# Performance work log

Measured on AMD Instinct MI355X. Metric: run time of the kernel, lower is better.

The kernel has to match this reference:

```python
import jax, jax.numpy as jnp
import numpy as np

L, D, H, FF, V = 8, 768, 8, 2048, 32000
MAXLEN, TMAX = 512, 4
S = MAXLEN * TMAX  # 2048 context length
HD = D // H
EPS = 1e-4  # layer_norm_eps from module defaults


def setup_inputs() -> dict:
    key = jax.random.key(0)
    ks = jax.random.split(key, 16)
    s = 0.02
    B = 1
    rn = lambda k, shape: jax.random.normal(k, shape, jnp.float32) * s
    # sinusoidal positional encoding over MAXLEN real-token positions
    pos = np.arange(MAXLEN)[:, None]
    div = np.exp(np.arange(0, D, 2) * (-np.log(10000.0) / D))
    pe = np.zeros((MAXLEN, D), np.float32)
    pe[:, 0::2] = np.sin(pos * div)
    pe[:, 1::2] = np.cos(pos * div)
    return {
        "state_embeddings": jax.random.normal(ks[0], (B, S, D), jnp.float32),
        "padding_mask": jnp.zeros((B, S), bool),
        "pe": jnp.asarray(pe),
        "thought_emb": rn(ks[1], (TMAX, D)),
        "w_qkv": rn(ks[2], (L, 3 * D, D)),
        "b_qkv": jnp.zeros((L, 3 * D), jnp.float32),
        "w_out": rn(ks[3], (L, D, D)),
        "b_out": jnp.zeros((L, D), jnp.float32),
        "ln1_g": jnp.ones((L, D), jnp.float32),
        "ln1_b": jnp.zeros((L, D), jnp.float32),
        "ln2_g": jnp.ones((L, D), jnp.float32),
        "ln2_b": jnp.zeros((L, D), jnp.float32),
        "w_ff1": rn(ks[4], (L, FF, D)),
        "b_ff1": jnp.zeros((L, FF), jnp.float32),
        "w_ff2": rn(ks[5], (L, D, FF)),
        "b_ff2": jnp.zeros((L, D), jnp.float32),
        "fn_g": jnp.ones((D,), jnp.float32),
        "fn_b": jnp.zeros((D,), jnp.float32),
        "w_policy": rn(ks[6], (V, D)),
        "w_v1": rn(ks[7], (FF, D)),
        "b_v1": jnp.zeros((FF,), jnp.float32),
        "w_v2": rn(ks[8], (1, FF)),
        "b_v2": jnp.zeros((1,), jnp.float32),
        "n_thoughts_taken": 3,
    }


def _layer_norm(x, g, b):
    m = x.mean(-1, keepdims=True)
    v = ((x - m) ** 2).mean(-1, keepdims=True)
    return (x - m) / jnp.sqrt(v + EPS) * g + b


def reference(state_embeddings, padding_mask, pe, thought_emb, w_qkv, b_qkv, w_out, b_out, ln1_g, ln1_b, ln2_g, ln2_b, w_ff1, b_ff1, w_ff2, b_ff2, fn_g, fn_b, w_policy, w_v1, b_v1, w_v2, b_v2, n_thoughts_taken):
    tt = int(n_thoughts_taken)
    T = tt + 1  # block size (token + thoughts taken)
    B = state_embeddings.shape[0]
    R = MAXLEN  # real_token_count: all token slots real (no padding)
    # --- DualPositionalEncoding ---
    x = state_embeddings[:, :MAXLEN * T].reshape(B, MAXLEN, T, D)
    x = x + pe[None, :, None, :] + thought_emb[None, None, :T, :]
    x = x.reshape(B, MAXLEN * T, D)
    x = jnp.pad(x, ((0, 0), (0, S - MAXLEN * T), (0, 0)))
    # --- ThoughtsFormer block-causal mask (keep=True means attend) ---
    i = jnp.arange(S)
    tok, off = i // T, i % T
    same_block = (tok[:, None] == tok[None, :]) & (off[:, None] >= off[None, :]) & (tok[:, None] < R)
    global_cols = (off[None, :] == 0) & (tok[None, :] < R) & (i[:, None] > i[None, :]) & (i[:, None] < R * T)
    keep = (same_block | global_cols)[None, None] & (~padding_mask)[:, None, None, :]
    scale = 1.0 / np.sqrt(HD)

    def layer(h, p):
        wq, bq, wo, bo, g1, b1, g2, b2, wf1, bf1, wf2, bf2 = p
        # pre-norm self-attention
        y = _layer_norm(h, g1, b1)
        q, k, v = jnp.split(y @ wq.T + bq, 3, axis=-1)
        q = q.reshape(B, S, H, HD)
        k = k.reshape(B, S, H, HD)
        v = v.reshape(B, S, H, HD)
        scores = jnp.einsum('bihd,bjhd->bhij', q, k) * scale
        attn = jax.nn.softmax(jnp.where(keep, scores, -jnp.inf), axis=-1)
        o = jnp.einsum('bhij,bjhd->bihd', attn, v).reshape(B, S, D)
        h = h + o @ wo.T + bo
        # pre-norm FFN with exact (erf) GELU
        y = _layer_norm(h, g2, b2)
        h = h + jax.nn.gelu(y @ wf1.T + bf1, approximate=False) @ wf2.T + bf2
        h = jnp.where(jnp.isnan(h), 0.0, h)
        return h, None

    x, _ = jax.lax.scan(layer, x, (w_qkv, b_qkv, w_out, b_out, ln1_g, ln1_b, ln2_g, ln2_b, w_ff1, b_ff1, w_ff2, b_ff2))
    x = _layer_norm(x, fn_g, fn_b)  # TransformerEncoder final norm
    logits = x @ w_policy.T  # policy head (no bias)
    values = jax.nn.gelu(x @ w_v1.T + b_v1, approximate=False) @ w_v2.T + b_v2
    return logits, values
```

## Files before the change

kernel.cpp:

```cpp
#include <hip/hip_runtime.h>
#include <math.h>

#define S_TOT 2048
#define DMODEL 768
#define QKVD 2304
#define NHEAD 8
#define HDIM 96
#define FFDIM 2048
#define VOCAB 32000
#define MAXLEN_C 512
#define POL_CHUNK 3200
#define VLT_LD 2080
#define NEG_BIG (-3.0e38f)
#define M_INIT (-1.0e30f)
#define QK_SCALE 0.10206207261596575f

typedef __bf16 bf16x8 __attribute__((ext_vector_type(8)));
typedef float f32x4 __attribute__((ext_vector_type(4)));
typedef unsigned short u16x8 __attribute__((ext_vector_type(8)));
typedef unsigned short u16x4 __attribute__((ext_vector_type(4)));

__device__ __forceinline__ float gelu_exact(float x) {
  return 0.5f * x * (1.0f + erff(x * 0.70710678118654752f));
}

__device__ __forceinline__ float bf2f(unsigned short u) {
  union { unsigned int i; float f; } v;
  v.i = ((unsigned int)u) << 16;
  return v.f;
}

__device__ __forceinline__ unsigned short f2bf(float f) {
  union { float f; unsigned int i; } v;
  v.f = f;
  unsigned int x = v.i;
  return (unsigned short)((x + 0x7fffu + ((x >> 16) & 1u)) >> 16);
}

__device__ __forceinline__ unsigned int pack2bf(float a, float b) {
  return (unsigned int)f2bf(a) | ((unsigned int)f2bf(b) << 16);
}

__device__ __forceinline__ void gload_lds16(const unsigned short* g, unsigned short* l) {
  __builtin_amdgcn_global_load_lds(
      (const __attribute__((address_space(1))) unsigned int*)g,
      (__attribute__((address_space(3))) unsigned int*)l, 16, 0, 0);
}

__global__ __launch_bounds__(256) void embed_kernel(
    const float* __restrict__ se, const float* __restrict__ pe,
    const float* __restrict__ th, const int* __restrict__ ntt,
    float* __restrict__ X) {
  int idx = blockIdx.x * 256 + threadIdx.x;
  if (idx >= S_TOT * DMODEL) return;
  int p = idx / DMODEL;
  int d = idx - p * DMODEL;
  int T = ntt[0] + 1;
  float v = 0.0f;
  if (p < MAXLEN_C * T) {
    v = se[idx] + pe[(p / T) * DMODEL + d] + th[(p % T) * DMODEL + d];
  }
  X[idx] = v;
}

__global__ __launch_bounds__(256) void ln_bf_kernel(
    const float* __restrict__ X, const float* __restrict__ g,
    const float* __restrict__ b, unsigned short* __restrict__ Y) {
  __shared__ float red[4];
  const int row = blockIdx.x;
  const int tid = threadIdx.x;
  const float* x = X + (size_t)row * DMODEL;
  float v0 = x[tid], v1 = x[tid + 256], v2 = x[tid + 512];
  float s = v0 + v1 + v2;
  for (int o = 32; o; o >>= 1) s += __shfl_xor(s, o);
  if ((tid & 63) == 0) red[tid >> 6] = s;
  __syncthreads();
  float mean = (red[0] + red[1] + red[2] + red[3]) * (1.0f / DMODEL);
  float d0 = v0 - mean, d1 = v1 - mean, d2 = v2 - mean;
  float s2 = d0 * d0 + d1 * d1 + d2 * d2;
  for (int o = 32; o; o >>= 1) s2 += __shfl_xor(s2, o);
  __syncthreads();
  if ((tid & 63) == 0) red[tid >> 6] = s2;
  __syncthreads();
  float var = (red[0] + red[1] + red[2] + red[3]) * (1.0f / DMODEL);
  float rstd = rsqrtf(var + 1e-4f);
  unsigned short* y = Y + (size_t)row * DMODEL;
  y[tid]       = f2bf(d0 * rstd * g[tid]       + b[tid]);
  y[tid + 256] = f2bf(d1 * rstd * g[tid + 256] + b[tid + 256]);
  y[tid + 512] = f2bf(d2 * rstd * g[tid + 512] + b[tid + 512]);
}

__global__ __launch_bounds__(256) void cvt_kernel(
    const float* __restrict__ s, unsigned short* __restrict__ d, int n) {
  int i = (blockIdx.x * 256 + threadIdx.x) * 4;
  if (i >= n) return;
  float4 v = *(const float4*)(s + i);
  u16x4 o;
  o[0] = f2bf(v.x); o[1] = f2bf(v.y); o[2] = f2bf(v.z); o[3] = f2bf(v.w);
  *(u16x4*)(d + i) = o;
}

__global__ __launch_bounds__(256) void cvt4_kernel(
    const float* __restrict__ s0, const float* __restrict__ s1,
    const float* __restrict__ s2, const float* __restrict__ s3,
    unsigned short* __restrict__ d0, unsigned short* __restrict__ d1,
    unsigned short* __restrict__ d2, unsigned short* __restrict__ d3,
    int n0, int n1, int n2, int n3) {
  int i = (blockIdx.x * 256 + threadIdx.x) * 4;
  const float* s;
  unsigned short* d;
  if (i < n0) { s = s0; d = d0; }
  else if (i < n0 + n1) { i -= n0; s = s1; d = d1; }
  else if (i < n0 + n1 + n2) { i -= n0 + n1; s = s2; d = d2; }
  else if (i < n0 + n1 + n2 + n3) { i -= n0 + n1 + n2; s = s3; d = d3; }
  else return;
  float4 v = *(const float4*)(s + i);
  u16x4 o;
  o[0] = f2bf(v.x); o[1] = f2bf(v.y); o[2] = f2bf(v.z); o[3] = f2bf(v.w);
  *(u16x4*)(d + i) = o;
}

__global__ __launch_bounds__(256) void cvt6_kernel(
    const float* __restrict__ s0, const float* __restrict__ s1,
    const float* __restrict__ s2, const float* __restrict__ s3,
    const float* __restrict__ s4, const float* __restrict__ s5,
    unsigned short* __restrict__ d0, unsigned short* __restrict__ d1,
    unsigned short* __restrict__ d2, unsigned short* __restrict__ d3,
    unsigned short* __restrict__ d4, unsigned short* __restrict__ d5,
    int n0, int n1, int n2, int n3, int n4, int n5) {
  int i = (blockIdx.x * 256 + threadIdx.x) * 4;
  const float* s;
  unsigned short* d;
  if (i < n0) { s = s0; d = d0; }
  else if (i < n0 + n1) { i -= n0; s = s1; d = d1; }
  else if (i < n0 + n1 + n2) { i -= n0 + n1; s = s2; d = d2; }
  else if (i < n0 + n1 + n2 + n3) { i -= n0 + n1 + n2; s = s3; d = d3; }
  else if (i < n0 + n1 + n2 + n3 + n4) { i -= n0 + n1 + n2 + n3; s = s4; d = d4; }
  else if (i < n0 + n1 + n2 + n3 + n4 + n5) { i -= n0 + n1 + n2 + n3 + n4; s = s5; d = d5; }
  else return;
  float4 v = *(const float4*)(s + i);
  u16x4 o;
  o[0] = f2bf(v.x); o[1] = f2bf(v.y); o[2] = f2bf(v.z); o[3] = f2bf(v.w);
  *(u16x4*)(d + i) = o;
}

__global__ __launch_bounds__(256) void gemm_bf16_kernel(
    const unsigned short* __restrict__ A, const unsigned short* __restrict__ B,
    const float* __restrict__ bias, const float* __restrict__ res,
    void* __restrict__ Cout, int M, int N, int K, int ldc, int act, int outbf) {
  __shared__ __align__(16) unsigned short As[128 * 32];
  __shared__ __align__(16) unsigned short Bs[128 * 32];
  const int t = threadIdx.x;
  const int w = t >> 6, l = t & 63;
  const int n0 = blockIdx.x * 128, i0 = blockIdx.y * 128;
  const int wr = w >> 1, wc = w & 1;
  const int lr = l & 15;
  const int koff = (l >> 4) * 8;

  f32x4 acc[4][4] = {};

  const int srow = t >> 2;
  const int scol = (t & 3) * 8;
  const unsigned short* Ag = A + (size_t)(i0 + srow) * K + scol;
  const unsigned short* Bg = B + (size_t)(n0 + srow) * K + scol;
  unsigned short* Alds0 = &As[(w << 9)];
  unsigned short* Alds1 = &As[2048 + (w << 9)];
  unsigned short* Blds0 = &Bs[(w << 9)];
  unsigned short* Blds1 = &Bs[2048 + (w << 9)];

  for (int k0 = 0; k0 < K; k0 += 32) {
    __syncthreads();
    gload_lds16(Ag + k0, Alds0);
    gload_lds16(Ag + (size_t)64 * K + k0, Alds1);
    gload_lds16(Bg + k0, Blds0);
    gload_lds16(Bg + (size_t)64 * K + k0, Blds1);
    __syncthreads();

    bf16x8 af[4], bfr[4];
#pragma unroll
    for (int fi = 0; fi < 4; ++fi)
      af[fi] = *(const bf16x8*)&As[(wr * 64 + fi * 16 + lr) * 32 + koff];
#pragma unroll
    for (int fj = 0; fj < 4; ++fj)
      bfr[fj] = *(const bf16x8*)&Bs[(wc * 64 + fj * 16 + lr) * 32 + koff];
#pragma unroll
    for (int fi = 0; fi < 4; ++fi)
#pragma unroll
      for (int fj = 0; fj < 4; ++fj)
        acc[fi][fj] = __builtin_amdgcn_mfma_f32_16x16x32_bf16(
            af[fi], bfr[fj], acc[fi][fj], 0, 0, 0);
  }

  float bcol[4];
#pragma unroll
  for (int fj = 0; fj < 4; ++fj)
    bcol[fj] = bias ? bias[n0 + wc * 64 + fj * 16 + lr] : 0.0f;

#pragma unroll
  for (int fi = 0; fi < 4; ++fi) {
#pragma unroll
    for (int reg = 0; reg < 4; ++reg) {
      const int i = i0 + wr * 64 + fi * 16 + (l >> 4) * 4 + reg;
      const size_t rowbase = (size_t)i * ldc;
#pragma unroll
      for (int fj = 0; fj < 4; ++fj) {
        const int n = n0 + wc * 64 + fj * 16 + lr;
        float z = acc[fi][fj][reg] + bcol[fj];
        if (act) z = gelu_exact(z);
        if (res) z += res[rowbase + n];
        if (outbf) ((unsigned short*)Cout)[rowbase + n] = f2bf(z);
        else       ((float*)Cout)[rowbase + n] = z;
      }
    }
  }
}

__global__ __launch_bounds__(256) void gemm64_bf16_kernel(
    const unsigned short* __restrict__ A, const unsigned short* __restrict__ B,
    const float* __restrict__ bias, const float* __restrict__ res,
    void* __restrict__ Cout, int M, int N, int K, int ldc, int act, int outbf) {
  __shared__ __align__(16) unsigned short As[2 * 64 * 32];
  __shared__ __align__(16) unsigned short Bs[2 * 64 * 32];
  const int t = threadIdx.x;
  const int w = t >> 6, l = t & 63;
  const int n0 = blockIdx.x * 64, i0 = blockIdx.y * 64;
  const int wr = w >> 1, wc = w & 1;
  const int lr = l & 15;
  const int koff = (l >> 4) * 8;

  f32x4 acc[2][2] = {};

  const int srow = t >> 2;
  const int scol = (t & 3) * 8;
  const unsigned short* Ag = A + (size_t)(i0 + srow) * K + scol;
  const unsigned short* Bg = B + (size_t)(n0 + srow) * K + scol;
  unsigned short* Alds0 = &As[(w << 9)];
  unsigned short* Alds1 = &As[2048 + (w << 9)];
  unsigned short* Blds0 = &Bs[(w << 9)];
  unsigned short* Blds1 = &Bs[2048 + (w << 9)];

  for (int k0 = 0; k0 < K; k0 += 64) {
    __syncthreads();
    gload_lds16(Ag + k0, Alds0);
    gload_lds16(Ag + k0 + 32, Alds1);
    gload_lds16(Bg + k0, Blds0);
    gload_lds16(Bg + k0 + 32, Blds1);
    __syncthreads();

    bf16x8 af[2][2], bfr[2][2];
#pragma unroll
    for (int fi = 0; fi < 2; ++fi)
#pragma unroll
      for (int kk = 0; kk < 2; ++kk)
        af[fi][kk] = *(const bf16x8*)&As[kk * 2048 + (wr * 32 + fi * 16 + lr) * 32 + koff];
#pragma unroll
    for (int fj = 0; fj < 2; ++fj)
#pragma unroll
      for (int kk = 0; kk < 2; ++kk)
        bfr[fj][kk] = *(const bf16x8*)&Bs[kk * 2048 + (wc * 32 + fj * 16 + lr) * 32 + koff];
#pragma unroll
    for (int fi = 0; fi < 2; ++fi)
#pragma unroll
      for (int fj = 0; fj < 2; ++fj)
#pragma unroll
        for (int kk = 0; kk < 2; ++kk)
          acc[fi][fj] = __builtin_amdgcn_mfma_f32_16x16x32_bf16(
              af[fi][kk], bfr[fj][kk], acc[fi][fj], 0, 0, 0);
  }

  float bcol[2];
#pragma unroll
  for (int fj = 0; fj < 2; ++fj)
    bcol[fj] = bias ? bias[n0 + wc * 32 + fj * 16 + lr] : 0.0f;

#pragma unroll
  for (int fi = 0; fi < 2; ++fi) {
#pragma unroll
    for (int reg = 0; reg < 4; ++reg) {
      const int i = i0 + wr * 32 + fi * 16 + (l >> 4) * 4 + reg;
      const size_t rowbase = (size_t)i * ldc;
#pragma unroll
      for (int fj = 0; fj < 2; ++fj) {
        const int n = n0 + wc * 32 + fj * 16 + lr;
        float z = acc[fi][fj][reg] + bcol[fj];
        if (act) z = gelu_exact(z);
        if (res) z += res[rowbase + n];
        if (outbf) ((unsigned short*)Cout)[rowbase + n] = f2bf(z);
        else       ((float*)Cout)[rowbase + n] = z;
      }
    }
  }
}

__global__ __launch_bounds__(256) void repack_kernel(
    const unsigned short* __restrict__ qkv, const int* __restrict__ ntt,
    unsigned short* __restrict__ Kg, unsigned short* __restrict__ Vgt,
    unsigned short* __restrict__ Vlt) {
  __shared__ unsigned short vt[64][104];
  const int pb = blockIdx.x * 64, h = blockIdx.y;
  const int T = ntt[0] + 1;
  const int tid = threadIdx.x;

  for (int idx = tid; idx < 64 * 96; idx += 256) {
    int pp = idx / 96, d = idx - pp * 96;
    vt[pp][d] = qkv[(size_t)(pb + pp) * QKVD + 2 * DMODEL + h * HDIM + d];
  }
  const int firstpp = (T - pb % T) % T;
  const int ng = (64 - firstpp + T - 1) / T;
  for (int idx = tid; idx < ng * 96; idx += 256) {
    int gi = idx / 96, d = idx - gi * 96;
    int p = pb + firstpp + gi * T;
    int g = p / T;
    if (g < MAXLEN_C)
      Kg[((size_t)h * 512 + g) * 96 + d] = qkv[(size_t)p * QKVD + DMODEL + h * HDIM + d];
  }
  __syncthreads();
  for (int idx = tid; idx < 96 * 64; idx += 256) {
    int d = idx >> 6, pp = idx & 63;
    Vlt[((size_t)h * 96 + d) * VLT_LD + pb + pp] = vt[pp][d];
  }
  for (int idx = tid; idx < ng * 96; idx += 256) {
    int d = idx / ng, gi = idx - d * ng;
    int pp = firstpp + gi * T;
    int g = (pb + pp) / T;
    if (g < MAXLEN_C && d < 96)
      Vgt[((size_t)h * 96 + d) * 512 + g] = vt[pp][d];
  }
}

__global__ __launch_bounds__(256) void attn_flash_kernel(
    const unsigned short* __restrict__ qkv, const unsigned short* __restrict__ Kg,
    const unsigned short* __restrict__ Vgt, const unsigned short* __restrict__ Vlt,
    const int* __restrict__ ntt, unsigned short* __restrict__ att) {
  __shared__ float Osh[4][96][17];
  __shared__ float Msh[4][16];
  __shared__ float Lsh[4][16];
  const int s = blockIdx.x, h = blockIdx.y;
  const int T = ntt[0] + 1;
  const int tid = threadIdx.x;
  const int w = tid >> 6, l = tid & 63;
  const int q15 = l & 15, grp = l >> 4;
  const int p0 = s * 16;
  const int p = p0 + q15;
  const int myTok = p / T;

  const unsigned short* qrow = qkv + (size_t)p * QKVD + h * HDIM + grp * 8;
  bf16x8 qf0 = *(const bf16x8*)(qrow);
  bf16x8 qf1 = *(const bf16x8*)(qrow + 32);
  bf16x8 qf2 = *(const bf16x8*)(qrow + 64);

  float m_run = M_INIT, l_run = 0.0f;
  f32x4 oacc[6] = {};

  const int gmax = (p0 + 15) / T;
  const int KP = (gmax >> 5) + 1;
  const unsigned short* KgH = Kg + (size_t)h * 512 * 96;
  const unsigned short* VgH = Vgt + (size_t)h * 96 * 512;

  for (int kp = w; kp < KP; kp += 4) {
    f32x4 s0 = {}, s1 = {};
    const unsigned short* k0r = KgH + (size_t)(kp * 32 + q15) * 96 + grp * 8;
    const unsigned short* k1r = k0r + 16 * 96;
    {
      bf16x8 a0 = *(const bf16x8*)(k0r);
      bf16x8 a1 = *(const bf16x8*)(k1r);
      s0 = __builtin_amdgcn_mfma_f32_16x16x32_bf16(a0, qf0, s0, 0, 0, 0);
      s1 = __builtin_amdgcn_mfma_f32_16x16x32_bf16(a1, qf0, s1, 0, 0, 0);
      a0 = *(const bf16x8*)(k0r + 32);
      a1 = *(const bf16x8*)(k1r + 32);
      s0 = __builtin_amdgcn_mfma_f32_16x16x32_bf16(a0, qf1, s0, 0, 0, 0);
      s1 = __builtin_amdgcn_mfma_f32_16x16x32_bf16(a1, qf1, s1, 0, 0, 0);
      a0 = *(const bf16x8*)(k0r + 64);
      a1 = *(const bf16x8*)(k1r + 64);
      s0 = __builtin_amdgcn_mfma_f32_16x16x32_bf16(a0, qf2, s0, 0, 0, 0);
      s1 = __builtin_amdgcn_mfma_f32_16x16x32_bf16(a1, qf2, s1, 0, 0, 0);
    }
    float sc[8];
#pragma unroll
    for (int e = 0; e < 4; ++e) {
      int g = kp * 32 + grp * 4 + e;
      sc[e] = (g * T <= p) ? s0[e] * QK_SCALE : NEG_BIG;
      g += 16;
      sc[4 + e] = (g * T <= p) ? s1[e] * QK_SCALE : NEG_BIG;
    }
    float tmax = sc[0];
#pragma unroll
    for (int e = 1; e < 8; ++e) tmax = fmaxf(tmax, sc[e]);
    tmax = fmaxf(tmax, __shfl_xor(tmax, 16));
    tmax = fmaxf(tmax, __shfl_xor(tmax, 32));
    float mnew = fmaxf(m_run, tmax);
    float alpha = __expf(m_run - mnew);
    float pv[8], ps = 0.0f;
#pragma unroll
    for (int e = 0; e < 8; ++e) { pv[e] = __expf(sc[e] - mnew); ps += pv[e]; }
    ps += __shfl_xor(ps, 16);
    ps += __shfl_xor(ps, 32);
    l_run = l_run * alpha + ps;
    m_run = mnew;
#pragma unroll
    for (int dt = 0; dt < 6; ++dt) oacc[dt] *= alpha;
    unsigned int pk0[2], pk1[2];
    pk0[0] = pack2bf(pv[0], pv[1]); pk0[1] = pack2bf(pv[2], pv[3]);
    pk1[0] = pack2bf(pv[4], pv[5]); pk1[1] = pack2bf(pv[6], pv[7]);
    union { unsigned int u[4]; bf16x8 v; } pf;
#pragma unroll
    for (int w2 = 0; w2 < 4; ++w2) {
      int src = (((grp & 1) << 1) + (w2 >> 1)) * 16 + q15;
      int y0 = __shfl((int)pk0[w2 & 1], src);
      int y1 = __shfl((int)pk1[w2 & 1], src);
      pf.u[w2] = (grp >> 1) ? (unsigned int)y1 : (unsigned int)y0;
    }
#pragma unroll
    for (int dt = 0; dt < 6; ++dt) {
      bf16x8 vf = *(const bf16x8*)(VgH + (size_t)(dt * 16 + q15) * 512 + kp * 32 + grp * 8);
      oacc[dt] = __builtin_amdgcn_mfma_f32_16x16x32_bf16(vf, pf.v, oacc[dt], 0, 0, 0);
    }
  }

  if (w == 3) {
    f32x4 s0 = {};
    const unsigned short* kl = qkv + (size_t)(p0 + q15) * QKVD + DMODEL + h * HDIM + grp * 8;
    s0 = __builtin_amdgcn_mfma_f32_16x16x32_bf16(*(const bf16x8*)(kl), qf0, s0, 0, 0, 0);
    s0 = __builtin_amdgcn_mfma_f32_16x16x32_bf16(*(const bf16x8*)(kl + 32), qf1, s0, 0, 0, 0);
    s0 = __builtin_amdgcn_mfma_f32_16x16x32_bf16(*(const bf16x8*)(kl + 64), qf2, s0, 0, 0, 0);
    float sc[4];
#pragma unroll
    for (int e = 0; e < 4; ++e) {
      int pk = p0 + grp * 4 + e;
      bool ok = (pk / T == myTok) && (pk % T != 0) && (pk <= p);
      sc[e] = ok ? s0[e] * QK_SCALE : NEG_BIG;
    }
    float tmax = fmaxf(fmaxf(sc[0], sc[1]), fmaxf(sc[2], sc[3]));
    tmax = fmaxf(tmax, __shfl_xor(tmax, 16));
    tmax = fmaxf(tmax, __shfl_xor(tmax, 32));
    float mnew = fmaxf(m_run, tmax);
    float alpha = __expf(m_run - mnew);
    float pv[4], ps = 0.0f;
#pragma unroll
    for (int e = 0; e < 4; ++e) { pv[e] = __expf(sc[e] - mnew); ps += pv[e]; }
    ps += __shfl_xor(ps, 16);
    ps += __shfl_xor(ps, 32);
    l_run = l_run * alpha + ps;
    m_run = mnew;
#pragma unroll
    for (int dt = 0; dt < 6; ++dt) oacc[dt] *= alpha;
    unsigned int pk0[2];
    pk0[0] = pack2bf(pv[0], pv[1]); pk0[1] = pack2bf(pv[2], pv[3]);
    union { unsigned int u[4]; bf16x8 v; } pf;
#pragma unroll
    for (int w2 = 0; w2 < 4; ++w2) {
      int src = (((grp & 1) << 1) + (w2 >> 1)) * 16 + q15;
      int y0 = __shfl((int)pk0[w2 & 1], src);
      pf.u[w2] = (grp >> 1) ? 0u : (unsigned int)y0;
    }
#pragma unroll
    for (int dt = 0; dt < 6; ++dt) {
      bf16x8 vf = *(const bf16x8*)(Vlt + ((size_t)h * 96 + dt * 16 + q15) * VLT_LD + p0 + grp * 8);
      oacc[dt] = __builtin_amdgcn_mfma_f32_16x16x32_bf16(vf, pf.v, oacc[dt], 0, 0, 0);
    }
  }

  if (l < 16) { Msh[w][l] = m_run; Lsh[w][l] = l_run; }
#pragma unroll
  for (int dt = 0; dt < 6; ++dt)
#pragma unroll
    for (int e = 0; e < 4; ++e)
      Osh[w][dt * 16 + grp * 4 + e][q15] = oacc[dt][e];
  __syncthreads();

  {
    const int q = tid & 15, dg = tid >> 4;
    float m0 = Msh[0][q], m1 = Msh[1][q], m2 = Msh[2][q], m3 = Msh[3][q];
    float ms = fmaxf(fmaxf(m0, m1), fmaxf(m2, m3));
    float c0 = __expf(m0 - ms), c1 = __expf(m1 - ms);
    float c2 = __expf(m2 - ms), c3 = __expf(m3 - ms);
    float lsum = c0 * Lsh[0][q] + c1 * Lsh[1][q] + c2 * Lsh[2][q] + c3 * Lsh[3][q];
    float rinv = 1.0f / lsum;
    unsigned short* orow = att + (size_t)(p0 + q) * DMODEL + h * HDIM;
#pragma unroll
    for (int j = 0; j < 6; ++j) {
      int d = dg * 6 + j;
      float o = c0 * Osh[0][d][q] + c1 * Osh[1][d][q] +
                c2 * Osh[2][d][q] + c3 * Osh[3][d][q];
      orow[d] = f2bf(o * rinv);
    }
  }
}

__global__ __launch_bounds__(256) void v2_kernel(
    const unsigned short* __restrict__ F1, const float* __restrict__ w2,
    const float* __restrict__ b2, float* __restrict__ out) {
  __shared__ float red[4];
  const int row = blockIdx.x;
  const int tid = threadIdx.x;
  float s = 0.0f;
  const unsigned short* xr = F1 + (size_t)row * FFDIM;
  for (int f = tid; f < FFDIM; f += 256) s += bf2f(xr[f]) * w2[f];
  for (int o = 32; o; o >>= 1) s += __shfl_xor(s, o);
  if ((tid & 63) == 0) red[tid >> 6] = s;
  __syncthreads();
  if (tid == 0) out[row] = red[0] + red[1] + red[2] + red[3] + b2[0];
}

extern "C" void kernel_launch(void* const* d_in, const int* in_sizes, int n_in,
                              void* d_out, int out_size, void* d_ws, size_t ws_size,
                              hipStream_t stream) {
  const float* se      = (const float*)d_in[0];
  const float* pe      = (const float*)d_in[2];
  const float* th      = (const float*)d_in[3];
  const float* w_qkv   = (const float*)d_in[4];
  const float* b_qkv   = (const float*)d_in[5];
  const float* w_out   = (const float*)d_in[6];
  const float* b_out   = (const float*)d_in[7];
  const float* ln1_g   = (const float*)d_in[8];
  const float* ln1_b   = (const float*)d_in[9];
  const float* ln2_g   = (const float*)d_in[10];
  const float* ln2_b   = (const float*)d_in[11];
  const float* w_ff1   = (const float*)d_in[12];
  const float* b_ff1   = (const float*)d_in[13];
  const float* w_ff2   = (const float*)d_in[14];
  const float* b_ff2   = (const float*)d_in[15];
  const float* fn_g    = (const float*)d_in[16];
  const float* fn_b    = (const float*)d_in[17];
  const float* w_pol   = (const float*)d_in[18];
  const float* w_v1    = (const float*)d_in[19];
  const float* b_v1    = (const float*)d_in[20];
  const float* w_v2    = (const float*)d_in[21];
  const float* b_v2    = (const float*)d_in[22];
  const int*   ntt     = (const int*)d_in[23];

  float* logits = (float*)d_out;
  float* values = logits + (size_t)S_TOT * VOCAB;

  const int nq = 3 * DMODEL * DMODEL, no = DMODEL * DMODEL;
  const int nf1 = FFDIM * DMODEL, nf2 = DMODEL * FFDIM;
  const int npol = VOCAB * DMODEL;

  char* p = (char*)d_ws;
  float* X             = (float*)p;          p += (size_t)S_TOT * DMODEL * 4;
  unsigned short* Ybf  = (unsigned short*)p; p += (size_t)S_TOT * DMODEL * 2;
  unsigned short* QKVb = (unsigned short*)p; p += (size_t)S_TOT * QKVD * 2;
  unsigned short* ATTb = (unsigned short*)p; p += (size_t)S_TOT * DMODEL * 2;
  unsigned short* F1b  = (unsigned short*)p; p += (size_t)S_TOT * FFDIM * 2;
  unsigned short* Kg   = (unsigned short*)p; p += (size_t)NHEAD * 512 * 96 * 2;
  unsigned short* Vgt  = (unsigned short*)p; p += (size_t)NHEAD * 96 * 512 * 2;
  unsigned short* Vlt  = (unsigned short*)p; p += (size_t)NHEAD * 96 * VLT_LD * 2;

  const size_t wbytes = ((size_t)8 * (nq + no + nf1 + nf2) + npol + nf1) * 2;
  const size_t used   = (size_t)(p - (char*)d_ws);
  const bool bigws = ws_size >= used + wbytes + (1u << 20);

  unsigned short *WqA, *WoA, *Wf1A, *Wf2A, *WpolA, *Wv1A;
  if (bigws) {
    WqA   = (unsigned short*)p; p += (size_t)8 * nq * 2;
    WoA   = (unsigned short*)p; p += (size_t)8 * no * 2;
    Wf1A  = (unsigned short*)p; p += (size_t)8 * nf1 * 2;
    Wf2A  = (unsigned short*)p; p += (size_t)8 * nf2 * 2;
    WpolA = (unsigned short*)p; p += (size_t)npol * 2;
    Wv1A  = (unsigned short*)p;
  } else {
    WqA   = (unsigned short*)p; p += (size_t)nq * 2;
    WoA   = (unsigned short*)p; p += (size_t)no * 2;
    Wf1A  = (unsigned short*)p; p += (size_t)nf1 * 2;
    Wf2A  = (unsigned short*)p; p += (size_t)nf2 * 2;
    WpolA = (unsigned short*)p;
    Wv1A  = Wf1A;
  }

  dim3 blk(256);

  if (bigws) {
    const int t0 = 8 * nq, t1 = 8 * no, t2 = 8 * nf1, t3 = 8 * nf2;
    const long total = (long)t0 + t1 + t2 + t3 + npol + nf1;
    cvt6_kernel<<<dim3((unsigned)((total / 4 + 255) / 256)), blk, 0, stream>>>(
        w_qkv, w_out, w_ff1, w_ff2, w_pol, w_v1,
        WqA, WoA, Wf1A, Wf2A, WpolA, Wv1A,
        t0, t1, t2, t3, npol, nf1);
  }

  embed_kernel<<<dim3((S_TOT * DMODEL + 255) / 256), blk, 0, stream>>>(se, pe, th, ntt, X);

  for (int l = 0; l < 8; ++l) {
    const unsigned short* pWq  = bigws ? WqA  + (size_t)l * nq  : WqA;
    const unsigned short* pWo  = bigws ? WoA  + (size_t)l * no  : WoA;
    const unsigned short* pWf1 = bigws ? Wf1A + (size_t)l * nf1 : Wf1A;
    const unsigned short* pWf2 = bigws ? Wf2A + (size_t)l * nf2 : Wf2A;
    if (!bigws) {
      const int ncvt4 = (nq + no + nf1 + nf2) / 4;
      cvt4_kernel<<<dim3((ncvt4 + 255) / 256), blk, 0, stream>>>(
          w_qkv + (size_t)l * nq, w_out + (size_t)l * no,
          w_ff1 + (size_t)l * nf1, w_ff2 + (size_t)l * nf2,
          WqA, WoA, Wf1A, Wf2A, nq, no, nf1, nf2);
    }

    ln_bf_kernel<<<dim3(S_TOT), blk, 0, stream>>>(X, ln1_g + l * DMODEL, ln1_b + l * DMODEL, Ybf);
    gemm_bf16_kernel<<<dim3(QKVD / 128, S_TOT / 128), blk, 0, stream>>>(
        Ybf, pWq, b_qkv + (size_t)l * 3 * DMODEL, nullptr, QKVb,
        S_TOT, QKVD, DMODEL, QKVD, 0, 1);
    repack_kernel<<<dim3(S_TOT / 64, NHEAD), blk, 0, stream>>>(QKVb, ntt, Kg, Vgt, Vlt);
    attn_flash_kernel<<<dim3(S_TOT / 16, NHEAD), blk, 0, stream>>>(
        QKVb, Kg, Vgt, Vlt, ntt, ATTb);
    gemm64_bf16_kernel<<<dim3(DMODEL / 64, S_TOT / 64), blk, 0, stream>>>(
        ATTb, pWo, b_out + (size_t)l * DMODEL, X, X,
        S_TOT, DMODEL, DMODEL, DMODEL, 0, 0);

    ln_bf_kernel<<<dim3(S_TOT), blk, 0, stream>>>(X, ln2_g + l * DMODEL, ln2_b + l * DMODEL, Ybf);
    gemm_bf16_kernel<<<dim3(FFDIM / 128, S_TOT / 128), blk, 0, stream>>>(
        Ybf, pWf1, b_ff1 + (size_t)l * FFDIM, nullptr, F1b,
        S_TOT, FFDIM, DMODEL, FFDIM, 1, 1);
    gemm64_bf16_kernel<<<dim3(DMODEL / 64, S_TOT / 64), blk, 0, stream>>>(
        F1b, pWf2, b_ff2 + (size_t)l * DMODEL, X, X,
        S_TOT, DMODEL, FFDIM, DMODEL, 0, 0);
  }

  ln_bf_kernel<<<dim3(S_TOT), blk, 0, stream>>>(X, fn_g, fn_b, Ybf);

  if (bigws) {
    gemm_bf16_kernel<<<dim3(VOCAB / 128, S_TOT / 128), blk, 0, stream>>>(
        Ybf, WpolA, nullptr, nullptr, logits, S_TOT, VOCAB, DMODEL, VOCAB, 0, 0);
  } else {
    for (int c = 0; c < VOCAB / POL_CHUNK; ++c) {
      cvt_kernel<<<dim3((POL_CHUNK * DMODEL / 4 + 255) / 256), blk, 0, stream>>>(
          w_pol + (size_t)c * POL_CHUNK * DMODEL, WpolA, POL_CHUNK * DMODEL);
      gemm_bf16_kernel<<<dim3(POL_CHUNK / 128, S_TOT / 128), blk, 0, stream>>>(
          Ybf, WpolA, nullptr, nullptr, logits + (size_t)c * POL_CHUNK,
          S_TOT, POL_CHUNK, DMODEL, VOCAB, 0, 0);
    }
  }

  if (!bigws)
    cvt_kernel<<<dim3((nf1 / 4 + 255) / 256), blk, 0, stream>>>(w_v1, Wv1A, nf1);
  gemm_bf16_kernel<<<dim3(FFDIM / 128, S_TOT / 128), blk, 0, stream>>>(
      Ybf, Wv1A, b_v1, nullptr, F1b, S_TOT, FFDIM, DMODEL, FFDIM, 1, 1);
  v2_kernel<<<dim3(S_TOT), blk, 0, stream>>>(F1b, w_v2, b_v2, values);
}
```

Measured before the change: 1.517 ms.

## Swizzle policy GEMM blocks across XCDs and prioritize MFMA in attention

The policy-head GEMM now runs on a 1D grid and remaps block IDs so consecutive blocks assigned round-robin to the 8 XCDs cover contiguous M-tiles of the same N column, which should improve L2 reuse of the weight and activation tiles. In the flash-attention kernel, all K fragment loads are hoisted ahead of the QK MFMAs, and s_setprio raises wave priority around the MFMA sequences to favour matrix issue over other waves. The swizzle hardcodes 16 M-tiles and assumes the grid divides by 8. The priority hints may help or hurt scheduling depending on occupancy.

```diff
diff --git a/kernel.cpp b/kernel.cpp
--- a/kernel.cpp
+++ b/kernel.cpp
@@ -147,12 +147,23 @@
 __global__ __launch_bounds__(256) void gemm_bf16_kernel(
     const unsigned short* __restrict__ A, const unsigned short* __restrict__ B,
     const float* __restrict__ bias, const float* __restrict__ res,
-    void* __restrict__ Cout, int M, int N, int K, int ldc, int act, int outbf) {
+    void* __restrict__ Cout, int M, int N, int K, int ldc, int act, int outbf,
+    int swiz) {
   __shared__ __align__(16) unsigned short As[128 * 32];
   __shared__ __align__(16) unsigned short Bs[128 * 32];
   const int t = threadIdx.x;
   const int w = t >> 6, l = t & 63;
-  const int n0 = blockIdx.x * 128, i0 = blockIdx.y * 128;
+  int n_blk, m_blk;
+  if (swiz) {
+    const int g = blockIdx.x;
+    const int chunk = gridDim.x >> 3;
+    const int logical = (g & 7) * chunk + (g >> 3);
+    m_blk = logical & 15;
+    n_blk = logical >> 4;
+  } else {
+    n_blk = blockIdx.x; m_blk = blockIdx.y;
+  }
+  const int n0 = n_blk * 128, i0 = m_blk * 128;
   const int wr = w >> 1, wc = w & 1;
   const int lr = l & 15;
   const int koff = (l >> 4) * 8;
@@ -364,16 +375,18 @@
     {
       bf16x8 a0 = *(const bf16x8*)(k0r);
       bf16x8 a1 = *(const bf16x8*)(k1r);
+      bf16x8 b0 = *(const bf16x8*)(k0r + 32);
+      bf16x8 b1 = *(const bf16x8*)(k1r + 32);
+      bf16x8 c0 = *(const bf16x8*)(k0r + 64);
+      bf16x8 c1 = *(const bf16x8*)(k1r + 64);
+      __builtin_amdgcn_s_setprio(1);
       s0 = __builtin_amdgcn_mfma_f32_16x16x32_bf16(a0, qf0, s0, 0, 0, 0);
       s1 = __builtin_amdgcn_mfma_f32_16x16x32_bf16(a1, qf0, s1, 0, 0, 0);
-      a0 = *(const bf16x8*)(k0r + 32);
-      a1 = *(const bf16x8*)(k1r + 32);
-      s0 = __builtin_amdgcn_mfma_f32_16x16x32_bf16(a0, qf1, s0, 0, 0, 0);
-      s1 = __builtin_amdgcn_mfma_f32_16x16x32_bf16(a1, qf1, s1, 0, 0, 0);
-      a0 = *(const bf16x8*)(k0r + 64);
-      a1 = *(const bf16x8*)(k1r + 64);
-      s0 = __builtin_amdgcn_mfma_f32_16x16x32_bf16(a0, qf2, s0, 0, 0, 0);
-      s1 = __builtin_amdgcn_mfma_f32_16x16x32_bf16(a1, qf2, s1, 0, 0, 0);
+      s0 = __builtin_amdgcn_mfma_f32_16x16x32_bf16(b0, qf1, s0, 0, 0, 0);
+      s1 = __builtin_amdgcn_mfma_f32_16x16x32_bf16(b1, qf1, s1, 0, 0, 0);
+      s0 = __builtin_amdgcn_mfma_f32_16x16x32_bf16(c0, qf2, s0, 0, 0, 0);
+      s1 = __builtin_amdgcn_mfma_f32_16x16x32_bf16(c1, qf2, s1, 0, 0, 0);
+      __builtin_amdgcn_s_setprio(0);
     }
     float sc[8];
 #pragma unroll
@@ -410,19 +423,23 @@
       int y1 = __shfl((int)pk1[w2 & 1], src);
       pf.u[w2] = (grp >> 1) ? (unsigned int)y1 : (unsigned int)y0;
     }
+    __builtin_amdgcn_s_setprio(1);
 #pragma unroll
     for (int dt = 0; dt < 6; ++dt) {
       bf16x8 vf = *(const bf16x8*)(VgH + (size_t)(dt * 16 + q15) * 512 + kp * 32 + grp * 8);
       oacc[dt] = __builtin_amdgcn_mfma_f32_16x16x32_bf16(vf, pf.v, oacc[dt], 0, 0, 0);
     }
+    __builtin_amdgcn_s_setprio(0);
   }
 
   if (w == 3) {
     f32x4 s0 = {};
     const unsigned short* kl = qkv + (size_t)(p0 + q15) * QKVD + DMODEL + h * HDIM + grp * 8;
+    __builtin_amdgcn_s_setprio(1);
     s0 = __builtin_amdgcn_mfma_f32_16x16x32_bf16(*(const bf16x8*)(kl), qf0, s0, 0, 0, 0);
     s0 = __builtin_amdgcn_mfma_f32_16x16x32_bf16(*(const bf16x8*)(kl + 32), qf1, s0, 0, 0, 0);
     s0 = __builtin_amdgcn_mfma_f32_16x16x32_bf16(*(const bf16x8*)(kl + 64), qf2, s0, 0, 0, 0);
+    __builtin_amdgcn_s_setprio(0);
     float sc[4];
 #pragma unroll
     for (int e = 0; e < 4; ++e) {
@@ -453,11 +470,13 @@
       int y0 = __shfl((int)pk0[w2 & 1], src);
       pf.u[w2] = (grp >> 1) ? 0u : (unsigned int)y0;
     }
+    __builtin_amdgcn_s_setprio(1);
 #pragma unroll
     for (int dt = 0; dt < 6; ++dt) {
       bf16x8 vf = *(const bf16x8*)(Vlt + ((size_t)h * 96 + dt * 16 + q15) * VLT_LD + p0 + grp * 8);
       oacc[dt] = __builtin_amdgcn_mfma_f32_16x16x32_bf16(vf, pf.v, oacc[dt], 0, 0, 0);
     }
+    __builtin_amdgcn_s_setprio(0);
   }
 
   if (l < 16) { Msh[w][l] = m_run; Lsh[w][l] = l_run; }
@@ -596,7 +615,7 @@
     ln_bf_kernel<<<dim3(S_TOT), blk, 0, stream>>>(X, ln1_g + l * DMODEL, ln1_b + l * DMODEL, Ybf);
     gemm_bf16_kernel<<<dim3(QKVD / 128, S_TOT / 128), blk, 0, stream>>>(
         Ybf, pWq, b_qkv + (size_t)l * 3 * DMODEL, nullptr, QKVb,
-        S_TOT, QKVD, DMODEL, QKVD, 0, 1);
+        S_TOT, QKVD, DMODEL, QKVD, 0, 1, 0);
     repack_kernel<<<dim3(S_TOT / 64, NHEAD), blk, 0, stream>>>(QKVb, ntt, Kg, Vgt, Vlt);
     attn_flash_kernel<<<dim3(S_TOT / 16, NHEAD), blk, 0, stream>>>(
         QKVb, Kg, Vgt, Vlt, ntt, ATTb);
@@ -607,7 +626,7 @@
     ln_bf_kernel<<<dim3(S_TOT), blk, 0, stream>>>(X, ln2_g + l * DMODEL, ln2_b + l * DMODEL, Ybf);
     gemm_bf16_kernel<<<dim3(FFDIM / 128, S_TOT / 128), blk, 0, stream>>>(
         Ybf, pWf1, b_ff1 + (size_t)l * FFDIM, nullptr, F1b,
-        S_TOT, FFDIM, DMODEL, FFDIM, 1, 1);
+        S_TOT, FFDIM, DMODEL, FFDIM, 1, 1, 0);
     gemm64_bf16_kernel<<<dim3(DMODEL / 64, S_TOT / 64), blk, 0, stream>>>(
         F1b, pWf2, b_ff2 + (size_t)l * DMODEL, X, X,
         S_TOT, DMODEL, FFDIM, DMODEL, 0, 0);
@@ -616,21 +635,21 @@
   ln_bf_kernel<<<dim3(S_TOT), blk, 0, stream>>>(X, fn_g, fn_b, Ybf);
 
   if (bigws) {
-    gemm_bf16_kernel<<<dim3(VOCAB / 128, S_TOT / 128), blk, 0, stream>>>(
-        Ybf, WpolA, nullptr, nullptr, logits, S_TOT, VOCAB, DMODEL, VOCAB, 0, 0);
+    gemm_bf16_kernel<<<dim3((S_TOT / 128) * (VOCAB / 128)), blk, 0, stream>>>(
+        Ybf, WpolA, nullptr, nullptr, logits, S_TOT, VOCAB, DMODEL, VOCAB, 0, 0, 1);
   } else {
     for (int c = 0; c < VOCAB / POL_CHUNK; ++c) {
       cvt_kernel<<<dim3((POL_CHUNK * DMODEL / 4 + 255) / 256), blk, 0, stream>>>(
           w_pol + (size_t)c * POL_CHUNK * DMODEL, WpolA, POL_CHUNK * DMODEL);
       gemm_bf16_kernel<<<dim3(POL_CHUNK / 128, S_TOT / 128), blk, 0, stream>>>(
           Ybf, WpolA, nullptr, nullptr, logits + (size_t)c * POL_CHUNK,
-          S_TOT, POL_CHUNK, DMODEL, VOCAB, 0, 0);
+          S_TOT, POL_CHUNK, DMODEL, VOCAB, 0, 0, 0);
     }
   }
 
   if (!bigws)
     cvt_kernel<<<dim3((nf1 / 4 + 255) / 256), blk, 0, stream>>>(w_v1, Wv1A, nf1);
   gemm_bf16_kernel<<<dim3(FFDIM / 128, S_TOT / 128), blk, 0, stream>>>(
-      Ybf, Wv1A, b_v1, nullptr, F1b, S_TOT, FFDIM, DMODEL, FFDIM, 1, 1);
+      Ybf, Wv1A, b_v1, nullptr, F1b, S_TOT, FFDIM, DMODEL, FFDIM, 1, 1, 0);
   v2_kernel<<<dim3(S_TOT), blk, 0, stream>>>(F1b, w_v2, b_v2, values);
 }
```

Result: no change. 1.524 ms (+0.5%).
